# Kernel optimization log

Hardware: AMD Instinct MI355X
Metric: run time of the kernel (lower is better)

Reference implementation:

```python
import jax, jax.numpy as jnp
import numpy as np

B, H, W, S = 4, 512, 512, 40
DZ = 0.1            # slice thickness
FOCUS_SLICE = 25    # back-propagation slice count
Z_PLANE = 2.0       # focus plane offset
PAD = 32            # output crop


def setup_inputs() -> dict:
    key = jax.random.key(0)
    ks = jax.random.split(key, 8)
    sample_re = jax.random.normal(ks[0], (B, H, W, S), jnp.float32) * 0.01
    sample_im = jax.random.normal(ks[1], (B, H, W, S), jnp.float32) * 0.01
    planewave_re = jax.random.normal(ks[2], (B, H, W), jnp.float32)
    planewave_im = jax.random.normal(ks[3], (B, H, W), jnp.float32)
    # kz strictly positive so 1/(2*kz) is finite (mask + nan-fix kept for faithfulness)
    kz = jax.random.uniform(ks[4], (H, W), jnp.float32) + 0.5
    otf_abs = jax.random.uniform(ks[5], (H, W), jnp.float32)
    green_mask = (jax.random.uniform(ks[6], (H, W), jnp.float32) < 0.7).astype(jnp.float32)
    otf_phase = jax.random.normal(ks[7], (H, W), jnp.float32) * 0.1
    return dict(sample_re=sample_re, sample_im=sample_im,
                planewave_re=planewave_re, planewave_im=planewave_im,
                kz=kz, otf_abs=otf_abs, green_mask=green_mask, otf_phase=otf_phase)


def reference(sample_re, sample_im, planewave_re, planewave_im, kz, otf_abs, green_mask, otf_phase):
    sample = (sample_re + 1j * sample_im).astype(jnp.complex64)        # [B,H,W,S]
    planewave = (planewave_re + 1j * planewave_im).astype(jnp.complex64)  # [B,H,W]
    kzc = kz.astype(jnp.complex64)

    # module constants: prop_kernel = exp(prop_kernel_pha * dz), prop_kernel_pha = 1j*kz
    prop_kernel = jnp.exp(1j * kzc * DZ)                               # [H,W]
    green = (1j * prop_kernel / (2.0 * kzc)) * green_mask.astype(jnp.complex64)
    green = jnp.where(jnp.isnan(green), jnp.zeros((), green.dtype), green)

    # _propegate_to_last_slice_Multi_Born (oblique_factor=None)
    inc0 = jnp.fft.fft2(planewave)                                     # fft over last two dims
    sample_s = jnp.moveaxis(sample, -1, 0)                             # [S,B,H,W]

    def step(inc, slab):
        u = inc * prop_kernel
        scat = green * jnp.fft.fft2(jnp.fft.ifft2(inc) * slab * DZ)
        return u + scat, None

    inc, _ = jax.lax.scan(step, inc0, sample_s)

    # _propegate_to_center_focus_slice
    pk_center = jnp.conj(prop_kernel ** FOCUS_SLICE)
    pk_focus = prop_kernel ** (Z_PLANE / DZ)
    inc = inc * pk_center * pk_focus

    # _pupil_constrain_abs_square_output with OTF_input provided
    otf_update = (otf_abs * jnp.exp(1j * otf_phase)).astype(jnp.complex64)
    out = jnp.fft.ifft2(inc * otf_update[None])
    return jnp.abs(out)[:, PAD:-PAD, PAD:-PAD]                          # [B, H-2*PAD, W-2*PAD]
```

## Files before the change

kernel.cpp:

```cpp
#include <hip/hip_runtime.h>
#include <hip/hip_fp16.h>
#include <math.h>

#define HW_ (512 * 512)

__device__ inline float2 cadd(float2 a, float2 b){ return make_float2(a.x+b.x, a.y+b.y); }
__device__ inline float2 csub(float2 a, float2 b){ return make_float2(a.x-b.x, a.y-b.y); }
__device__ inline float2 cmulf(float2 a, float2 b){ return make_float2(a.x*b.x-a.y*b.y, a.x*b.y+a.y*b.x); }
__device__ inline float bf2f(unsigned short u){ return __uint_as_float(((unsigned int)u) << 16); }
__device__ inline unsigned short f2bf(float f){
    unsigned int x = __float_as_uint(f);
    x += 0x7fffu + ((x >> 16) & 1u);
    return (unsigned short)(x >> 16);
}

template<bool INV>
__device__ inline void dft8(const float2 a[8], float2 X[8]) {
    const float C = 0.70710678118654752440f;
    float2 t0 = cadd(a[0], a[4]), t4 = csub(a[0], a[4]);
    float2 t1 = cadd(a[1], a[5]), d1 = csub(a[1], a[5]);
    float2 t2 = cadd(a[2], a[6]), d2 = csub(a[2], a[6]);
    float2 t3 = cadd(a[3], a[7]), d3 = csub(a[3], a[7]);
    float2 t5, t6, t7;
    if (!INV) {
        t5 = make_float2(C*(d1.x + d1.y), C*(d1.y - d1.x));
        t6 = make_float2(d2.y, -d2.x);
        t7 = make_float2(C*(d3.y - d3.x), -C*(d3.x + d3.y));
    } else {
        t5 = make_float2(C*(d1.x - d1.y), C*(d1.y + d1.x));
        t6 = make_float2(-d2.y, d2.x);
        t7 = make_float2(-C*(d3.x + d3.y), C*(d3.x - d3.y));
    }
    float2 u0 = cadd(t0, t2), u2 = csub(t0, t2);
    float2 u1 = cadd(t1, t3), e3 = csub(t1, t3);
    float2 u3 = INV ? make_float2(-e3.y, e3.x) : make_float2(e3.y, -e3.x);
    float2 u4 = cadd(t4, t6), u6 = csub(t4, t6);
    float2 u5 = cadd(t5, t7), e7 = csub(t5, t7);
    float2 u7 = INV ? make_float2(-e7.y, e7.x) : make_float2(e7.y, -e7.x);
    X[0] = cadd(u0, u1); X[4] = csub(u0, u1);
    X[2] = cadd(u2, u3); X[6] = csub(u2, u3);
    X[1] = cadd(u4, u5); X[5] = csub(u4, u5);
    X[3] = cadd(u6, u7); X[7] = csub(u6, u7);
}

template<bool INV>
__device__ inline void fft512_reg(float2 a[8], float2* __restrict__ xch,
                                  int lane, float2 T1, float2 T2)
{
    float2 tw1 = INV ? make_float2(T1.x, -T1.y) : T1;
    float2 tw2 = INV ? make_float2(T2.x, -T2.y) : T2;
    const int rdo = lane + (lane >> 3);
    float2 b[8];

    dft8<INV>(a, b);
    { float2 w = tw1;
      #pragma unroll
      for (int k = 1; k < 8; ++k) { b[k] = cmulf(b[k], w); w = cmulf(w, tw1); } }
    #pragma unroll
    for (int k = 0; k < 8; ++k) xch[9*lane + k] = b[k];
    __asm__ volatile("s_waitcnt lgkmcnt(0)" ::: "memory");
    #pragma unroll
    for (int j = 0; j < 8; ++j) a[j] = xch[rdo + 72*j];

    dft8<INV>(a, b);
    { float2 w = tw2;
      #pragma unroll
      for (int k = 1; k < 8; ++k) { b[k] = cmulf(b[k], w); w = cmulf(w, tw2); } }
    { const int wbase = (lane & 7) + 72 * (lane >> 3);
      #pragma unroll
      for (int k = 0; k < 8; ++k) xch[wbase + 9*k] = b[k]; }
    __asm__ volatile("s_waitcnt lgkmcnt(0)" ::: "memory");
    #pragma unroll
    for (int j = 0; j < 8; ++j) b[j] = xch[rdo + 72*j];

    dft8<INV>(b, a);
}

__global__ __launch_bounds__(256)
void k_pre(const float* __restrict__ kz, const float* __restrict__ otfa,
           const float* __restrict__ gmask, const float* __restrict__ otfp,
           float2* __restrict__ propT, float2* __restrict__ greenT,
           float2* __restrict__ MT)
{
    __shared__ float2 tp[32*33], tg[32*33], tm[32*33];
    const int tid = threadIdx.x;
    const int w0 = (blockIdx.x & 15) << 5;
    const int h0 = (blockIdx.x >> 4) << 5;
    const int ww = tid & 31, hh = tid >> 5;
    #pragma unroll
    for (int p = 0; p < 4; ++p) {
        int h = hh + p*8;
        int idx = (h0 + h)*512 + w0 + ww;
        float k = kz[idx];
        float sn, cs; __sincosf(k * 0.1f, &sn, &cs);
        float inv2 = 0.5f / k * gmask[idx];
        float phase = otfp[idx] - k * 0.5f;
        float s2, c2; __sincosf(phase, &s2, &c2);
        float oa = otfa[idx];
        tp[h*33 + ww] = make_float2(cs, sn);
        tg[h*33 + ww] = make_float2(-sn*inv2, cs*inv2);
        tm[h*33 + ww] = make_float2(oa*c2, oa*s2);
    }
    __syncthreads();
    #pragma unroll
    for (int p = 0; p < 4; ++p) {
        int wrow = hh + p*8;
        size_t o = (size_t)(w0 + wrow)*512 + h0 + ww;
        propT[o]  = tp[ww*33 + wrow];
        greenT[o] = tg[ww*33 + wrow];
        MT[o]     = tm[ww*33 + wrow];
    }
}

__global__ __launch_bounds__(256)
void k_transpose(const float* __restrict__ sre, const float* __restrict__ sim,
                 ushort2* __restrict__ sampT)
{
    __shared__ __align__(16) ushort2 tile[40 * 128];
    const int bh = blockIdx.x >> 2;
    const int chunk = blockIdx.x & 3;
    const int b = bh >> 9, h = bh & 511;
    const int w0 = chunk << 7;
    const float4* sre4 = (const float4*)(sre + (size_t)bh * 20480) + chunk * 1280;
    const float4* sim4 = (const float4*)(sim + (size_t)bh * 20480) + chunk * 1280;
    #pragma unroll
    for (int i = 0; i < 5; ++i) {
        int j = threadIdx.x + (i << 8);
        float4 re = sre4[j];
        float4 im = sim4[j];
        int w = j / 10;
        int m = j - w * 10;
        ushort2* row = &tile[(m << 2) * 128 + (w ^ ((m & 7) << 2))];
        row[0]   = make_ushort2(f2bf(re.x), f2bf(im.x));
        row[128] = make_ushort2(f2bf(re.y), f2bf(im.y));
        row[256] = make_ushort2(f2bf(re.z), f2bf(im.z));
        row[384] = make_ushort2(f2bf(re.w), f2bf(im.w));
    }
    __syncthreads();
    #pragma unroll
    for (int i = 0; i < 5; ++i) {
        int j = threadIdx.x + (i << 8);
        int s = j >> 5, q = j & 31;
        int qp = q ^ ((s >> 2) & 7);
        uint4 v = *(const uint4*)&tile[(s << 7) + (qp << 2)];
        *(uint4*)&sampT[(((size_t)s * 4 + b) * 512 + h) * 512 + w0 + (q << 2)] = v;
    }
}

__global__ __launch_bounds__(256)
void k_row(float2* __restrict__ fldA,
           ushort2* __restrict__ fld2,
           const float* __restrict__ pwre, const float* __restrict__ pwim,
           const ushort2* __restrict__ sampT,
           float* __restrict__ finout,
           int mode, int slice)
{
    __shared__ float2 xchall[4 * 576];
    const int tid = threadIdx.x, lane = tid & 63, wv = tid >> 6;
    float2* xch = &xchall[wv * 576];
    float s1, c1, s2, c2;
    __sincosf(-6.2831853071795864769f * (float)lane / 512.0f, &s1, &c1);
    __sincosf(-6.2831853071795864769f * (float)(lane >> 3) / 64.0f, &s2, &c2);
    const float2 T1 = make_float2(c1, s1), T2 = make_float2(c2, s2);

    const int r = blockIdx.x * 4 + wv;
    int b, h;
    if (mode == 2) { b = r / 448; h = 32 + (r - b * 448); }
    else           { b = r >> 9;  h = r & 511; }
    const size_t rbase = ((size_t)b * 512 + h) * 512;
    float2 a[8];

    if (mode == 0) {
        #pragma unroll
        for (int j = 0; j < 8; ++j) {
            int w = lane + (j << 6);
            a[j] = make_float2(pwre[rbase + w], pwim[rbase + w]);
        }
        fft512_reg<false>(a, xch, lane, T1, T2);
        #pragma unroll
        for (int j = 0; j < 8; ++j) fldA[rbase + lane + (j << 6)] = a[j];
        return;
    }

    #pragma unroll
    for (int j = 0; j < 8; ++j) a[j] = fldA[rbase + lane + (j << 6)];
    fft512_reg<true>(a, xch, lane, T1, T2);

    if (mode == 2) {
        float* orow = finout + ((size_t)b * 448 + (h - 32)) * 448;
        #pragma unroll
        for (int j = 0; j < 8; ++j) {
            int w = lane + (j << 6);
            if (w >= 32 && w < 480) {
                float2 v = a[j];
                orow[w - 32] = sqrtf(v.x*v.x + v.y*v.y) * (1.0f / 512.0f);
            }
        }
        return;
    }

    const float scale = 0.1f / 512.0f;
    const size_t sbase = (((size_t)slice * 4 + b) * 512 + h) * 512;
    #pragma unroll
    for (int j = 0; j < 8; ++j) {
        int w = lane + (j << 6);
        ushort2 u = sampT[sbase + w];
        float sr = bf2f(u.x), si = bf2f(u.y);
        float2 v = a[j];
        a[j] = make_float2((v.x*sr - v.y*si) * scale, (v.x*si + v.y*sr) * scale);
    }
    fft512_reg<false>(a, xch, lane, T1, T2);
    #pragma unroll
    for (int j = 0; j < 8; ++j) {
        float2 v = a[j];
        fld2[rbase + lane + (j << 6)] =
            make_ushort2(__half_as_ushort(__float2half(v.x)),
                         __half_as_ushort(__float2half(v.y)));
    }
}

__global__ __launch_bounds__(512)
void k_col(float2* __restrict__ fldA,
           const ushort2* __restrict__ fld2,
           const float2* __restrict__ propT, const float2* __restrict__ greenT,
           const float2* __restrict__ MT, int last)
{
    __shared__ float2 tileA[512 * 9];
    __shared__ ushort2 tile2[512 * 9];
    const int tid = threadIdx.x;
    const int lane = tid & 63, wv = tid >> 6;
    const int b = blockIdx.x >> 6;
    const int w0 = (blockIdx.x & 63) << 3;
    const int c = tid & 7, hb = tid >> 3;
    const size_t gbase = (size_t)b * HW_ + w0;

    float s1, c1, s2, c2;
    __sincosf(-6.2831853071795864769f * (float)lane / 512.0f, &s1, &c1);
    __sincosf(-6.2831853071795864769f * (float)(lane >> 3) / 64.0f, &s2, &c2);
    const float2 T1 = make_float2(c1, s1), T2 = make_float2(c2, s2);

    #pragma unroll
    for (int j = 0; j < 8; ++j) {
        int h = hb + (j << 6);
        tileA[h*9 + c] = fldA[gbase + (size_t)h * 512 + c];
        tile2[h*9 + c] = fld2[gbase + (size_t)h * 512 + c];
    }
    __syncthreads();
    float2 aA[8], aS[8];
    #pragma unroll
    for (int j = 0; j < 8; ++j) {
        int idx = (lane + (j << 6)) * 9 + wv;
        aA[j] = tileA[idx];
        ushort2 u = tile2[idx];
        aS[j] = make_float2(__half2float(__ushort_as_half(u.x)),
                            __half2float(__ushort_as_half(u.y)));
    }
    __syncthreads();
    float2* xch = &tileA[wv * 576];

    fft512_reg<false>(aA, xch, lane, T1, T2);
    fft512_reg<false>(aS, xch, lane, T1, T2);

    const int w = w0 + wv;
    const size_t pbase = (size_t)w * 512;
    #pragma unroll
    for (int k = 0; k < 8; ++k) {
        int h = lane + (k << 6);
        float2 p  = propT[pbase + h];
        float2 g  = greenT[pbase + h];
        float2 nw = make_float2(p.x*aA[k].x - p.y*aA[k].y + g.x*aS[k].x - g.y*aS[k].y,
                                p.x*aA[k].y + p.y*aA[k].x + g.x*aS[k].y + g.y*aS[k].x);
        if (last) nw = cmulf(nw, MT[pbase + h]);
        aA[k] = nw;
    }

    fft512_reg<true>(aA, xch, lane, T1, T2);
    __syncthreads();
    const float inv = 1.0f / 512.0f;
    #pragma unroll
    for (int k = 0; k < 8; ++k)
        tileA[(lane + (k << 6)) * 9 + wv] = make_float2(aA[k].x * inv, aA[k].y * inv);
    __syncthreads();
    #pragma unroll
    for (int j = 0; j < 8; ++j) {
        int h = hb + (j << 6);
        fldA[gbase + (size_t)h * 512 + c] = tileA[h*9 + c];
    }
}

extern "C" void kernel_launch(void* const* d_in, const int* in_sizes, int n_in,
                              void* d_out, int out_size, void* d_ws, size_t ws_size,
                              hipStream_t stream)
{
    (void)in_sizes; (void)n_in; (void)out_size; (void)ws_size;
    const float* sre   = (const float*)d_in[0];
    const float* simg  = (const float*)d_in[1];
    const float* pwre  = (const float*)d_in[2];
    const float* pwim  = (const float*)d_in[3];
    const float* kz    = (const float*)d_in[4];
    const float* otfa  = (const float*)d_in[5];
    const float* gmask = (const float*)d_in[6];
    const float* otfp  = (const float*)d_in[7];

    char* ws = (char*)d_ws;
    size_t off = 0;
    float2* propT  = (float2*)(ws + off); off += (size_t)HW_ * 8;
    float2* greenT = (float2*)(ws + off); off += (size_t)HW_ * 8;
    float2* MT     = (float2*)(ws + off); off += (size_t)HW_ * 8;
    float2* fldA   = (float2*)(ws + off); off += (size_t)4 * HW_ * 8;
    ushort2* fld2  = (ushort2*)(ws + off); off += (size_t)4 * HW_ * 4;
    ushort2* sampT = (ushort2*)(ws + off);

    k_pre<<<256, 256, 0, stream>>>(kz, otfa, gmask, otfp, propT, greenT, MT);
    k_transpose<<<8192, 256, 0, stream>>>(sre, simg, sampT);

    k_row<<<512, 256, 0, stream>>>(fldA, nullptr, pwre, pwim, nullptr, nullptr, 0, 0);

    for (int s = 0; s < 40; ++s) {
        k_row<<<512, 256, 0, stream>>>(fldA, fld2, nullptr, nullptr, sampT, nullptr, 1, s);
        k_col<<<256, 512, 0, stream>>>(fldA, fld2, propT, greenT, MT, (s == 39) ? 1 : 0);
    }
    k_row<<<448, 256, 0, stream>>>(fldA, nullptr, nullptr, nullptr, nullptr, (float*)d_out, 2, 0);
}
```

Measured before the change: 1.259 ms.

## Fuse per-slice row/column FFT kernels into one persistent cooperative kernel

```diff
diff --git a/kernel.cpp b/kernel.cpp
--- a/kernel.cpp
+++ b/kernel.cpp
@@ -1,6 +1,9 @@
 #include <hip/hip_runtime.h>
 #include <hip/hip_fp16.h>
+#include <hip/hip_cooperative_groups.h>
 #include <math.h>
+
+namespace cg = cooperative_groups;
 
 #define HW_ (512 * 512)
 
@@ -147,144 +150,157 @@
     }
 }
 
-__global__ __launch_bounds__(256)
-void k_row(float2* __restrict__ fldA,
-           ushort2* __restrict__ fld2,
-           const float* __restrict__ pwre, const float* __restrict__ pwim,
-           const ushort2* __restrict__ sampT,
-           float* __restrict__ finout,
-           int mode, int slice)
-{
-    __shared__ float2 xchall[4 * 576];
+__global__ __launch_bounds__(512, 2)
+void k_loop(float2* __restrict__ fldA, ushort2* __restrict__ fld2,
+            const float* __restrict__ pwre, const float* __restrict__ pwim,
+            const ushort2* __restrict__ sampT,
+            const float2* __restrict__ propT, const float2* __restrict__ greenT,
+            const float2* __restrict__ MT, float* __restrict__ out)
+{
+    cg::grid_group grid = cg::this_grid();
+    __shared__ float2  bufA[512 * 9];
+    __shared__ ushort2 buf2[512 * 9];
+
     const int tid = threadIdx.x, lane = tid & 63, wv = tid >> 6;
-    float2* xch = &xchall[wv * 576];
+    const int bk = blockIdx.x;
+    float2* xch = &bufA[wv * 576];
+
     float s1, c1, s2, c2;
     __sincosf(-6.2831853071795864769f * (float)lane / 512.0f, &s1, &c1);
     __sincosf(-6.2831853071795864769f * (float)(lane >> 3) / 64.0f, &s2, &c2);
     const float2 T1 = make_float2(c1, s1), T2 = make_float2(c2, s2);
 
-    const int r = blockIdx.x * 4 + wv;
-    int b, h;
-    if (mode == 2) { b = r / 448; h = 32 + (r - b * 448); }
-    else           { b = r >> 9;  h = r & 511; }
-    const size_t rbase = ((size_t)b * 512 + h) * 512;
+    const int rrow = bk * 8 + wv;
+    const int rb = rrow >> 9, rh = rrow & 511;
+    const size_t rbase = ((size_t)rb * 512 + rh) * 512;
+    const int cb = bk >> 6, w0 = (bk & 63) << 3;
+    const int w = w0 + wv;
+    const size_t cgbase = (size_t)cb * HW_ + w0;
+    const int cc = tid & 7, chb = tid >> 3;
+    const size_t pbase = (size_t)w * 512;
+
+    float2 inc[8], pr[8], gr[8];
+    #pragma unroll
+    for (int k = 0; k < 8; ++k) {
+        pr[k] = propT[pbase + lane + (k << 6)];
+        gr[k] = greenT[pbase + lane + (k << 6)];
+    }
+
     float2 a[8];
 
-    if (mode == 0) {
-        #pragma unroll
-        for (int j = 0; j < 8; ++j) {
-            int w = lane + (j << 6);
-            a[j] = make_float2(pwre[rbase + w], pwim[rbase + w]);
+    #pragma unroll
+    for (int j = 0; j < 8; ++j) {
+        int ww = lane + (j << 6);
+        a[j] = make_float2(pwre[rbase + ww], pwim[rbase + ww]);
+    }
+    fft512_reg<false>(a, xch, lane, T1, T2);
+    #pragma unroll
+    for (int j = 0; j < 8; ++j) fldA[rbase + lane + (j << 6)] = a[j];
+    grid.sync();
+
+    #pragma unroll
+    for (int j = 0; j < 8; ++j) {
+        int h = chb + (j << 6);
+        bufA[h*9 + cc] = fldA[cgbase + (size_t)h * 512 + cc];
+    }
+    __syncthreads();
+    #pragma unroll
+    for (int j = 0; j < 8; ++j) inc[j] = bufA[(lane + (j << 6)) * 9 + wv];
+    __syncthreads();
+    fft512_reg<false>(inc, xch, lane, T1, T2);
+    __syncthreads();
+
+    ushort2 smp[8];
+    {
+        const size_t sb0 = (((size_t)0 * 4 + rb) * 512 + rh) * 512;
+        #pragma unroll
+        for (int j = 0; j < 8; ++j) smp[j] = sampT[sb0 + lane + (j << 6)];
+    }
+
+    const float scale = 0.1f / 512.0f;
+    const float inv = 1.0f / 512.0f;
+
+    for (int s = 0; s < 40; ++s) {
+        #pragma unroll
+        for (int j = 0; j < 8; ++j) a[j] = fldA[rbase + lane + (j << 6)];
+        fft512_reg<true>(a, xch, lane, T1, T2);
+        #pragma unroll
+        for (int j = 0; j < 8; ++j) {
+            float sr = bf2f(smp[j].x), si = bf2f(smp[j].y);
+            float2 v = a[j];
+            a[j] = make_float2((v.x*sr - v.y*si) * scale, (v.x*si + v.y*sr) * scale);
+        }
+        if (s < 39) {
+            const size_t sbn = (((size_t)(s+1) * 4 + rb) * 512 + rh) * 512;
+            #pragma unroll
+            for (int j = 0; j < 8; ++j) smp[j] = sampT[sbn + lane + (j << 6)];
         }
         fft512_reg<false>(a, xch, lane, T1, T2);
         #pragma unroll
-        for (int j = 0; j < 8; ++j) fldA[rbase + lane + (j << 6)] = a[j];
-        return;
-    }
-
-    #pragma unroll
-    for (int j = 0; j < 8; ++j) a[j] = fldA[rbase + lane + (j << 6)];
-    fft512_reg<true>(a, xch, lane, T1, T2);
-
-    if (mode == 2) {
-        float* orow = finout + ((size_t)b * 448 + (h - 32)) * 448;
-        #pragma unroll
-        for (int j = 0; j < 8; ++j) {
-            int w = lane + (j << 6);
-            if (w >= 32 && w < 480) {
+        for (int j = 0; j < 8; ++j) {
+            float2 v = a[j];
+            fld2[rbase + lane + (j << 6)] =
+                make_ushort2(__half_as_ushort(__float2half(v.x)),
+                             __half_as_ushort(__float2half(v.y)));
+        }
+        grid.sync();
+
+        #pragma unroll
+        for (int j = 0; j < 8; ++j) {
+            int h = chb + (j << 6);
+            buf2[h*9 + cc] = fld2[cgbase + (size_t)h * 512 + cc];
+        }
+        __syncthreads();
+        #pragma unroll
+        for (int j = 0; j < 8; ++j) {
+            ushort2 u = buf2[(lane + (j << 6)) * 9 + wv];
+            a[j] = make_float2(__half2float(__ushort_as_half(u.x)),
+                               __half2float(__ushort_as_half(u.y)));
+        }
+        fft512_reg<false>(a, xch, lane, T1, T2);
+        #pragma unroll
+        for (int k = 0; k < 8; ++k) {
+            float2 nw = make_float2(
+                pr[k].x*inc[k].x - pr[k].y*inc[k].y + gr[k].x*a[k].x - gr[k].y*a[k].y,
+                pr[k].x*inc[k].y + pr[k].y*inc[k].x + gr[k].x*a[k].y + gr[k].y*a[k].x);
+            inc[k] = nw;
+        }
+        if (s == 39) {
+            #pragma unroll
+            for (int k = 0; k < 8; ++k) inc[k] = cmulf(inc[k], MT[pbase + lane + (k << 6)]);
+        }
+        #pragma unroll
+        for (int k = 0; k < 8; ++k) a[k] = inc[k];
+        fft512_reg<true>(a, xch, lane, T1, T2);
+        __syncthreads();
+        #pragma unroll
+        for (int k = 0; k < 8; ++k)
+            bufA[(lane + (k << 6)) * 9 + wv] = make_float2(a[k].x * inv, a[k].y * inv);
+        __syncthreads();
+        #pragma unroll
+        for (int j = 0; j < 8; ++j) {
+            int h = chb + (j << 6);
+            fldA[cgbase + (size_t)h * 512 + cc] = bufA[h*9 + cc];
+        }
+        grid.sync();
+    }
+
+    if (wv < 7) {
+        const int r = bk * 7 + wv;
+        const int ob = r / 448, oh = r - ob * 448;
+        const size_t fbase = ((size_t)ob * 512 + oh + 32) * 512;
+        #pragma unroll
+        for (int j = 0; j < 8; ++j) a[j] = fldA[fbase + lane + (j << 6)];
+        fft512_reg<true>(a, xch, lane, T1, T2);
+        float* orow = out + ((size_t)ob * 448 + oh) * 448;
+        #pragma unroll
+        for (int j = 0; j < 8; ++j) {
+            int ww = lane + (j << 6);
+            if (ww >= 32 && ww < 480) {
                 float2 v = a[j];
-                orow[w - 32] = sqrtf(v.x*v.x + v.y*v.y) * (1.0f / 512.0f);
+                orow[ww - 32] = sqrtf(v.x*v.x + v.y*v.y) * (1.0f / 512.0f);
             }
         }
-        return;
-    }
-
-    const float scale = 0.1f / 512.0f;
-    const size_t sbase = (((size_t)slice * 4 + b) * 512 + h) * 512;
-    #pragma unroll
-    for (int j = 0; j < 8; ++j) {
-        int w = lane + (j << 6);
-        ushort2 u = sampT[sbase + w];
-        float sr = bf2f(u.x), si = bf2f(u.y);
-        float2 v = a[j];
-        a[j] = make_float2((v.x*sr - v.y*si) * scale, (v.x*si + v.y*sr) * scale);
-    }
-    fft512_reg<false>(a, xch, lane, T1, T2);
-    #pragma unroll
-    for (int j = 0; j < 8; ++j) {
-        float2 v = a[j];
-        fld2[rbase + lane + (j << 6)] =
-            make_ushort2(__half_as_ushort(__float2half(v.x)),
-                         __half_as_ushort(__float2half(v.y)));
-    }
-}
-
-__global__ __launch_bounds__(512)
-void k_col(float2* __restrict__ fldA,
-           const ushort2* __restrict__ fld2,
-           const float2* __restrict__ propT, const float2* __restrict__ greenT,
-           const float2* __restrict__ MT, int last)
-{
-    __shared__ float2 tileA[512 * 9];
-    __shared__ ushort2 tile2[512 * 9];
-    const int tid = threadIdx.x;
-    const int lane = tid & 63, wv = tid >> 6;
-    const int b = blockIdx.x >> 6;
-    const int w0 = (blockIdx.x & 63) << 3;
-    const int c = tid & 7, hb = tid >> 3;
-    const size_t gbase = (size_t)b * HW_ + w0;
-
-    float s1, c1, s2, c2;
-    __sincosf(-6.2831853071795864769f * (float)lane / 512.0f, &s1, &c1);
-    __sincosf(-6.2831853071795864769f * (float)(lane >> 3) / 64.0f, &s2, &c2);
-    const float2 T1 = make_float2(c1, s1), T2 = make_float2(c2, s2);
-
-    #pragma unroll
-    for (int j = 0; j < 8; ++j) {
-        int h = hb + (j << 6);
-        tileA[h*9 + c] = fldA[gbase + (size_t)h * 512 + c];
-        tile2[h*9 + c] = fld2[gbase + (size_t)h * 512 + c];
-    }
-    __syncthreads();
-    float2 aA[8], aS[8];
-    #pragma unroll
-    for (int j = 0; j < 8; ++j) {
-        int idx = (lane + (j << 6)) * 9 + wv;
-        aA[j] = tileA[idx];
-        ushort2 u = tile2[idx];
-        aS[j] = make_float2(__half2float(__ushort_as_half(u.x)),
-                            __half2float(__ushort_as_half(u.y)));
-    }
-    __syncthreads();
-    float2* xch = &tileA[wv * 576];
-
-    fft512_reg<false>(aA, xch, lane, T1, T2);
-    fft512_reg<false>(aS, xch, lane, T1, T2);
-
-    const int w = w0 + wv;
-    const size_t pbase = (size_t)w * 512;
-    #pragma unroll
-    for (int k = 0; k < 8; ++k) {
-        int h = lane + (k << 6);
-        float2 p  = propT[pbase + h];
-        float2 g  = greenT[pbase + h];
-        float2 nw = make_float2(p.x*aA[k].x - p.y*aA[k].y + g.x*aS[k].x - g.y*aS[k].y,
-                                p.x*aA[k].y + p.y*aA[k].x + g.x*aS[k].y + g.y*aS[k].x);
-        if (last) nw = cmulf(nw, MT[pbase + h]);
-        aA[k] = nw;
-    }
-
-    fft512_reg<true>(aA, xch, lane, T1, T2);
-    __syncthreads();
-    const float inv = 1.0f / 512.0f;
-    #pragma unroll
-    for (int k = 0; k < 8; ++k)
-        tileA[(lane + (k << 6)) * 9 + wv] = make_float2(aA[k].x * inv, aA[k].y * inv);
-    __syncthreads();
-    #pragma unroll
-    for (int j = 0; j < 8; ++j) {
-        int h = hb + (j << 6);
-        fldA[gbase + (size_t)h * 512 + c] = tileA[h*9 + c];
     }
 }
 
@@ -310,15 +326,14 @@
     float2* fldA   = (float2*)(ws + off); off += (size_t)4 * HW_ * 8;
     ushort2* fld2  = (ushort2*)(ws + off); off += (size_t)4 * HW_ * 4;
     ushort2* sampT = (ushort2*)(ws + off);
+    float* outp    = (float*)d_out;
 
     k_pre<<<256, 256, 0, stream>>>(kz, otfa, gmask, otfp, propT, greenT, MT);
     k_transpose<<<8192, 256, 0, stream>>>(sre, simg, sampT);
 
-    k_row<<<512, 256, 0, stream>>>(fldA, nullptr, pwre, pwim, nullptr, nullptr, 0, 0);
-
-    for (int s = 0; s < 40; ++s) {
-        k_row<<<512, 256, 0, stream>>>(fldA, fld2, nullptr, nullptr, sampT, nullptr, 1, s);
-        k_col<<<256, 512, 0, stream>>>(fldA, fld2, propT, greenT, MT, (s == 39) ? 1 : 0);
-    }
-    k_row<<<448, 256, 0, stream>>>(fldA, nullptr, nullptr, nullptr, nullptr, (float*)d_out, 2, 0);
-}
+    void* kargs[] = { (void*)&fldA, (void*)&fld2, (void*)&pwre, (void*)&pwim,
+                      (void*)&sampT, (void*)&propT, (void*)&greenT, (void*)&MT,
+                      (void*)&outp };
+    hipLaunchCooperativeKernel((const void*)k_loop, dim3(256), dim3(512),
+                               kargs, 0, stream);
+}
```

Result: slower. 3.478 ms (+176.4%).
